# Optimization experiments

Measured on AMD Instinct MI355X. Metric: run time of the kernel, lower is better.

## Reference

```python
import math
import jax, jax.numpy as jnp
import numpy as np

# --- Cayley-Dickson octonion structure constants: e_i * e_j = sign * e_{i XOR j} ---
def _cd_tables(levels=3):
    idx = np.array([[0]]); sgn = np.array([[1]])
    for _ in range(levels):
        n = idx.shape[0]; N = 2 * n
        I = np.zeros((N, N), np.int64); S = np.zeros((N, N), np.int64)
        cj = lambda j: 1 if j == 0 else -1  # conj sign of basis element j
        for i in range(n):
            for j in range(n):
                I[i, j] = idx[i, j];             S[i, j] = sgn[i, j]
                I[i, n + j] = n + idx[j, i];     S[i, n + j] = sgn[j, i]
                I[n + i, j] = n + idx[i, j];     S[n + i, j] = sgn[i, j] * cj(j)
                I[n + i, n + j] = idx[j, i];     S[n + i, n + j] = -cj(j) * sgn[j, i]
        idx, sgn = I, S
    return idx, sgn

_OIDX, _OSGN = _cd_tables()
# Octonion-structured linear: out_i = sum_j SIGN[i,j] * x_j @ W[WIDX[i,j]], WIDX[i,j]=i^j
_WIDX = np.array([[i ^ j for j in range(8)] for i in range(8)], np.int64)
_SIGN = np.array([[_OSGN[j, i ^ j] for j in range(8)] for i in range(8)], np.float32)


def _oct_linear(x, W):
    # x: [B,T,C], W: [8, C/8, C/8]
    B, T, C = x.shape
    Cp = C // 8
    parts = x.reshape(B, T, 8, Cp)
    Weff = jnp.asarray(_SIGN)[:, :, None, None] * W[jnp.asarray(_WIDX)]  # [8,8,Cp,Cp]
    return jnp.einsum('btjp,ijpq->btiq', parts, Weff).reshape(B, T, C)


def _rope(x, cos, sin):
    # x: [B,T,H,D]; consecutive channel pairs form complex numbers
    B, T, H, D = x.shape
    xr = x.reshape(B, T, H, D // 2, 2)
    xe, xo = xr[..., 0], xr[..., 1]
    c = cos[None, :, None, :]
    s = sin[None, :, None, :]
    return jnp.stack([xe * c - xo * s, xe * s + xo * c], axis=-1).reshape(B, T, H, D)


def _forward(x, Wq, Wk, Wv, Wo, mixer_W, mixer_beta, freqs_cos, freqs_sin):
    B, T, C = x.shape
    H = 32; D = C // H
    q = _oct_linear(x, Wq).reshape(B, T, H, D)
    k = _oct_linear(x, Wk).reshape(B, T, H, D)
    v = _oct_linear(x, Wv).reshape(B, T, H, D)
    q = _rope(q, freqs_cos, freqs_sin)
    k = _rope(k, freqs_cos, freqs_sin)
    q = q.transpose(0, 2, 1, 3)  # [B,H,T,D]
    k = k.transpose(0, 2, 1, 3)
    v = v.transpose(0, 2, 1, 3)
    scores = jnp.einsum('bhqd,bhkd->bhqk', q, k) / jnp.sqrt(jnp.float32(D))
    mask = jnp.tril(jnp.ones((T, T), bool))
    scores = jnp.where(mask, scores, jnp.finfo(scores.dtype).min)
    y = jnp.einsum('bhqk,bhkd->bhqd', jax.nn.softmax(scores, axis=-1), v)  # [B,H,T,D]
    # octonion head mixing in groups of 8 heads
    G = H // 8
    yg = y.reshape(B, G, 8, T, D)
    Weff = jnp.asarray(_SIGN)[:, :, None, None] * mixer_W[jnp.asarray(_WIDX)]  # [8,8,D,D]
    mixed = jnp.einsum('bgjtd,ijde->bgite', yg, Weff) * mixer_beta
    y = mixed.reshape(B, H, T, D).transpose(0, 2, 1, 3).reshape(B, T, C)
    return _oct_linear(y, Wo)


def setup_inputs() -> dict:
    key = jax.random.key(0)
    ks = jax.random.split(key, 8)
    B, T, C, H = 1, 2048, 4096, 32
    D = C // H; Cp = C // 8
    x = jax.random.normal(ks[0], (B, T, C), jnp.float32)
    Wq = jax.random.normal(ks[1], (8, Cp, Cp), jnp.float32) * 0.02
    Wk = jax.random.normal(ks[2], (8, Cp, Cp), jnp.float32) * 0.02
    Wv = jax.random.normal(ks[3], (8, Cp, Cp), jnp.float32) * 0.02
    Wo = jax.random.normal(ks[4], (8, Cp, Cp), jnp.float32) * 0.02
    mixer_W = jax.random.normal(ks[5], (8, D, D), jnp.float32) * 0.02
    mixer_beta = jnp.ones((D,), jnp.float32) * np.float32(math.sqrt(3.0 / (2.0 * D)))
    half = D // 2
    inv = 1.0 / (10000.0 ** (np.arange(half) * 2.0 / D))
    ang = np.arange(T)[:, None] * inv[None, :]
    freqs_cos = jnp.asarray(np.cos(ang), jnp.float32)
    freqs_sin = jnp.asarray(np.sin(ang), jnp.float32)
    return dict(x=x, Wq=Wq, Wk=Wk, Wv=Wv, Wo=Wo, mixer_W=mixer_W,
                mixer_beta=mixer_beta, freqs_cos=freqs_cos, freqs_sin=freqs_sin)


def reference(x, Wq, Wk, Wv, Wo, mixer_W, mixer_beta, freqs_cos, freqs_sin):
    return _forward(x, Wq, Wk, Wv, Wo, mixer_W, mixer_beta, freqs_cos, freqs_sin)
```

## Files before the change

kernel.cpp:

```cpp
#include <hip/hip_runtime.h>

typedef float f32x4 __attribute__((ext_vector_type(4)));
typedef __bf16 bf16x8 __attribute__((ext_vector_type(8)));
typedef unsigned short u16;
typedef u16 u16x8 __attribute__((ext_vector_type(8)));

__constant__ float c_osgn[64] = {
  1, 1, 1, 1, 1, 1, 1, 1,
  1,-1, 1,-1, 1,-1,-1, 1,
  1,-1,-1, 1, 1, 1,-1,-1,
  1, 1,-1,-1, 1,-1, 1,-1,
  1,-1,-1,-1,-1, 1, 1, 1,
  1, 1,-1, 1,-1,-1,-1, 1,
  1, 1, 1,-1,-1, 1,-1,-1,
  1,-1, 1, 1,-1,-1, 1,-1
};

__device__ __forceinline__ u16 f2bf(float f) {
  union { float f; unsigned u; } v; v.f = f;
  unsigned u = v.u;
  return (u16)((u + 0x7fffu + ((u >> 16) & 1u)) >> 16);
}
__device__ __forceinline__ float bf2f(u16 h) {
  union { unsigned u; float f; } v; v.u = ((unsigned)h) << 16;
  return v.f;
}

typedef const __attribute__((address_space(1))) void* as1cv;
typedef __attribute__((address_space(3))) void* as3v;
__device__ __forceinline__ void load16_lds(const void* g, void* l) {
  __builtin_amdgcn_global_load_lds((as1cv)g, (as3v)l, 16, 0, 0);
}

__global__ void conv_f32_bf16_vec(const float* __restrict__ src, u16* __restrict__ dst) {
  int i = blockIdx.x * 256 + threadIdx.x;
  float4 v = ((const float4*)src)[i];
  ushort4 o; o.x = f2bf(v.x); o.y = f2bf(v.y); o.z = f2bf(v.z); o.w = f2bf(v.w);
  ((ushort4*)dst)[i] = o;
}

__global__ __launch_bounds__(256) void transpose_w2(const float* __restrict__ W,
                                                    u16* __restrict__ Wt) {
  __shared__ float t[64][65];
  const int w = blockIdx.z, p0 = blockIdx.y * 64, q0 = blockIdx.x * 64;
  const float* src = W + ((long)w * 512 + p0) * 512 + q0;
  const int tid = threadIdx.x;
  const int r = tid >> 2, c0 = (tid & 3) * 16;
#pragma unroll
  for (int j = 0; j < 4; j++) {
    float4 v = *(const float4*)(src + (long)r * 512 + c0 + j * 4);
    t[r][c0 + j * 4 + 0] = v.x; t[r][c0 + j * 4 + 1] = v.y;
    t[r][c0 + j * 4 + 2] = v.z; t[r][c0 + j * 4 + 3] = v.w;
  }
  __syncthreads();
  u16* dst = Wt + ((long)w * 512 + q0) * 512 + p0;
#pragma unroll
  for (int j = 0; j < 2; j++) {
    u16x8 o;
#pragma unroll
    for (int k = 0; k < 8; k++) o[k] = f2bf(t[c0 + j * 8 + k][r]);
    *(u16x8*)(dst + (long)r * 512 + c0 + j * 8) = o;
  }
}

__global__ void transpose_wm(const float* __restrict__ W, const float* __restrict__ beta,
                             u16* __restrict__ Wt) {
  int idx = blockIdx.x * 256 + threadIdx.x;
  int w = idx >> 14, rem = idx & 16383;
  int e = rem >> 7, d = rem & 127;
  Wt[(w << 14) + (e << 7) + d] = f2bf(W[(w << 14) + (d << 7) + e] * beta[e]);
}

template <int MODE>
__global__ __launch_bounds__(256, 3) void oct_gemm128(
    const u16* __restrict__ A, const u16* __restrict__ WtB,
    void* __restrict__ out0, void* __restrict__ out1, void* __restrict__ out2,
    const float* __restrict__ fc, const float* __restrict__ fs,
    int K, int lda, int ldo,
    int slab_shift, int bs_shift, long wslab, long oslab, long acolslab)
{
  __shared__ u16 As[128][64];
  __shared__ u16 Bs[128][64];
  const int NT = K >> 6;
  const int BS = 1 << bs_shift;
  const long wblk = (long)BS * BS;

  const int nwg = gridDim.x * gridDim.y;
  const int lin = blockIdx.y * gridDim.x + blockIdx.x;
  const int swz = (lin & 7) * (nwg >> 3) + (lin >> 3);
  const int bx = swz % gridDim.x, by = swz / gridDim.x;

  const int nglob = bx * 128;
  const int z = nglob >> slab_shift;
  const int np = nglob & ((1 << slab_shift) - 1);
  const int bi = np >> bs_shift;
  const int nsub = np & (BS - 1);
  const int bm = by * 128;
  const u16* Wt = WtB + (long)z * wslab;
  const long acol0 = (long)z * acolslab;

  const int tid = threadIdx.x;
  const int lane = tid & 63, w = tid >> 6;
  const int l15 = lane & 15, lg = lane >> 4;
  const int wm = w >> 1, wn = w & 1;
  const int srow = lane >> 3;
  const int sgr  = (lane & 7) ^ srow;

  f32x4 acc[4][4];
#pragma unroll
  for (int a = 0; a < 4; a++)
#pragma unroll
    for (int b = 0; b < 4; b++) acc[a][b] = f32x4{0.f, 0.f, 0.f, 0.f};

  for (int t = 0; t < NT; ++t) {
    const int k0 = t << 6;
    const int bj = k0 >> bs_shift;
    const int widx = bi ^ bj;
    const unsigned xm = (c_osgn[bj * 8 + widx] < 0.f) ? 0x80008000u : 0u;
    const u16* Wsrc = Wt + (long)widx * wblk + (k0 & (BS - 1));

#pragma unroll
    for (int i = 0; i < 4; i++) {
      const int r = (w * 4 + i) * 8;
      load16_lds(A + (long)(bm + r + srow) * lda + acol0 + k0 + sgr * 8,
                 (void*)&As[r][0]);
    }
#pragma unroll
    for (int i = 0; i < 4; i++) {
      const int r = (w * 4 + i) * 8;
      load16_lds(Wsrc + (long)(nsub + r + srow) * BS + sgr * 8,
                 (void*)&Bs[r][0]);
    }
    __syncthreads();

#pragma unroll
    for (int kk = 0; kk < 64; kk += 32) {
      const int gsw = (((kk >> 3) + lg) ^ (l15 & 7)) * 8;
      uint4 a4[4];
      bf16x8 bF[4];
#pragma unroll
      for (int mt = 0; mt < 4; mt++)
        a4[mt] = *(const uint4*)&As[wm * 64 + mt * 16 + l15][gsw];
      if (xm) {
#pragma unroll
        for (int mt = 0; mt < 4; mt++) {
          a4[mt].x ^= xm; a4[mt].y ^= xm; a4[mt].z ^= xm; a4[mt].w ^= xm;
        }
      }
#pragma unroll
      for (int nt = 0; nt < 4; nt++)
        bF[nt] = *(const bf16x8*)&Bs[wn * 64 + nt * 16 + l15][gsw];
#pragma unroll
      for (int mt = 0; mt < 4; mt++)
#pragma unroll
        for (int nt = 0; nt < 4; nt++)
          acc[mt][nt] = __builtin_amdgcn_mfma_f32_16x16x32_bf16(
              *(const bf16x8*)&a4[mt], bF[nt], acc[mt][nt], 0, 0, 0);
    }
    __syncthreads();
  }

  if constexpr (MODE == 1) {
    if (z == 2) {
      u16* vg = (u16*)out2;
#pragma unroll
      for (int mt = 0; mt < 4; mt++)
#pragma unroll
        for (int nt = 0; nt < 4; nt++)
#pragma unroll
          for (int j = 0; j < 4; j++) {
            const int row = bm + wm * 64 + mt * 16 + 4 * lg + j;
            const int col = np + wn * 64 + nt * 16 + l15;
            vg[(long)row * 4096 + col] = f2bf(acc[mt][nt][j]);
          }
    } else {
      u16* dq = (u16*)(z == 0 ? out0 : out1);
      const int h = np >> 7;
#pragma unroll
      for (int mt = 0; mt < 4; mt++)
#pragma unroll
        for (int nt = 0; nt < 4; nt++) {
          const int d = wn * 64 + nt * 16 + l15;
          const int p = d >> 1;
          const bool ev = (l15 & 1) == 0;
#pragma unroll
          for (int j = 0; j < 4; j++) {
            const int trow = bm + wm * 64 + mt * 16 + 4 * lg + j;
            const float v = acc[mt][nt][j];
            const float sh = __shfl_xor(v, 1);
            const float c = fc[trow * 64 + p];
            const float s = fs[trow * 64 + p];
            const float o = ev ? (v * c - sh * s) : (sh * s + v * c);
            dq[((long)h * 2048 + trow) * 128 + d] = f2bf(o);
          }
        }
    }
  } else {
#pragma unroll
    for (int mt = 0; mt < 4; mt++)
#pragma unroll
      for (int nt = 0; nt < 4; nt++)
#pragma unroll
        for (int j = 0; j < 4; j++) {
          const int row = bm + wm * 64 + mt * 16 + 4 * lg + j;
          const int col = np + wn * 64 + nt * 16 + l15;
          const float v = acc[mt][nt][j];
          if constexpr (MODE == 0)
            ((u16*)out0)[(long)z * oslab + (long)row * ldo + col] = f2bf(v);
          else
            ((float*)out0)[(long)row * ldo + col] = v;
        }
  }
}

__global__ void v_transpose(const u16* __restrict__ vg, u16* __restrict__ vT)
{
  int h = blockIdx.x, t0 = blockIdx.y * 64;
  __shared__ u16 lds[64][136];
  int tid = threadIdx.x;
  int rr = tid >> 4, ch = (tid & 15) * 8;
#pragma unroll
  for (int p = 0; p < 4; p++) {
    int row = p * 16 + rr;
    *(uint4*)&lds[row][ch] = *(const uint4*)(vg + (long)(t0 + row) * 4096 + h * 128 + ch);
  }
  __syncthreads();
  int dd = tid >> 3, tc = (tid & 7) * 8;
#pragma unroll
  for (int p = 0; p < 4; p++) {
    int d = p * 32 + dd;
    u16x8 o;
#pragma unroll
    for (int j = 0; j < 8; j++) o[j] = lds[tc + j][d];
    *(u16x8*)(vT + ((long)h * 128 + d) * 2048 + t0 + tc) = o;
  }
}

__global__ __launch_bounds__(256, 2) void attn3(
    const u16* __restrict__ qR, const u16* __restrict__ kR,
    const u16* __restrict__ vT, u16* __restrict__ y)
{
  const int bid = blockIdx.x;
  const int h = bid & 31;
  const int u = bid >> 5;
  const int qb = (u < 8) ? (u * 2) : (31 - u * 2);
  const int q0 = qb * 128;

  const int tid = threadIdx.x;
  const int lane = tid & 63, w = tid >> 6;
  const int l15 = lane & 15, lg = lane >> 4;

  __shared__ u16 Ks[2][64][128];
  __shared__ u16 Vs[2][128][64];
  __shared__ u16 Ps[4][32][64];

  auto stageK = [&](int kb, int buf) {
    const long kbase = (long)h * 2048 + (long)kb * 64;
#pragma unroll
    for (int i = 0; i < 4; i++) {
      const int j = w * 4 + i;
      const int row = j * 4 + (lane >> 4);
      const int sg = (lane & 15) ^ (row & 7);
      load16_lds(kR + (kbase + row) * 128 + sg * 8, (void*)&Ks[buf][j * 4][0]);
    }
  };
  auto stageV = [&](int kb, int buf) {
    const long vbase = (long)h * 128 * 2048 + (long)kb * 64;
#pragma unroll
    for (int i = 0; i < 4; i++) {
      const int j = w * 4 + i;
      const int row = j * 8 + (lane >> 3);
      const int sg = (lane & 7) ^ (row & 7);
      load16_lds(vT + vbase + (long)row * 2048 + sg * 8, (void*)&Vs[buf][j * 8][0]);
    }
  };

  stageK(0, 0);
  stageV(0, 0);

  bf16x8 aQ[2][4];
#pragma unroll
  for (int rs = 0; rs < 2; rs++) {
    const long qbase = ((long)h * 2048 + q0 + w * 32 + rs * 16 + l15) * 128;
#pragma unroll
    for (int c = 0; c < 4; c++)
      aQ[rs][c] = *(const bf16x8*)(qR + qbase + 32 * c + 8 * lg);
  }

  float m[2][4], lsum[2][4];
  f32x4 Y[2][8];
#pragma unroll
  for (int rs = 0; rs < 2; rs++)
#pragma unroll
    for (int rr = 0; rr < 4; rr++) { m[rs][rr] = -1e30f; lsum[rs][rr] = 0.f; }
#pragma unroll
  for (int rs = 0; rs < 2; rs++)
#pragma unroll
    for (int dt = 0; dt < 8; dt++) Y[rs][dt] = f32x4{0.f, 0.f, 0.f, 0.f};

  const float scale = 0.08838834764831845f;
  const int nkb = 2 * qb + 2;

  for (int kb = 0; kb < nkb; kb++) {
    const int buf = kb & 1;
    const int k0 = kb * 64;
    if (kb + 1 < nkb) { stageK(kb + 1, buf ^ 1); stageV(kb + 1, buf ^ 1); }
    if (kb + 1 < nkb) asm volatile("s_waitcnt vmcnt(8)" ::: "memory");
    else              asm volatile("s_waitcnt vmcnt(0)" ::: "memory");
    __builtin_amdgcn_s_barrier();
    asm volatile("" ::: "memory");

    f32x4 S[2][4];
#pragma unroll
    for (int rs = 0; rs < 2; rs++)
#pragma unroll
      for (int ks = 0; ks < 4; ks++) S[rs][ks] = f32x4{0.f, 0.f, 0.f, 0.f};
#pragma unroll
    for (int c = 0; c < 4; c++) {
      bf16x8 bK[4];
#pragma unroll
      for (int ks = 0; ks < 4; ks++)
        bK[ks] = *(const bf16x8*)&Ks[buf][ks * 16 + l15][(((4 * c + lg) ^ (l15 & 7)) * 8)];
#pragma unroll
      for (int rs = 0; rs < 2; rs++)
#pragma unroll
        for (int ks = 0; ks < 4; ks++)
          S[rs][ks] = __builtin_amdgcn_mfma_f32_16x16x32_bf16(aQ[rs][c], bK[ks], S[rs][ks], 0, 0, 0);
    }

#pragma unroll
    for (int rs = 0; rs < 2; rs++) {
      const int qrow0 = q0 + w * 32 + rs * 16 + 4 * lg;
#pragma unroll
      for (int ks = 0; ks < 4; ks++) {
        const int kg = k0 + ks * 16 + l15;
#pragma unroll
        for (int rr = 0; rr < 4; rr++) {
          float s = S[rs][ks][rr] * scale;
          S[rs][ks][rr] = (kg > qrow0 + rr) ? -1e30f : s;
        }
      }
      float sf[4];
      bool need = false;
#pragma unroll
      for (int rr = 0; rr < 4; rr++) {
        float mx = fmaxf(fmaxf(S[rs][0][rr], S[rs][1][rr]),
                         fmaxf(S[rs][2][rr], S[rs][3][rr]));
#pragma unroll
        for (int off = 1; off < 16; off <<= 1) mx = fmaxf(mx, __shfl_xor(mx, off));
        const bool upd = (mx > m[rs][rr] + 8.f);
        const float mn = upd ? mx : m[rs][rr];
        const float sc = upd ? __expf(m[rs][rr] - mn) : 1.f;
        need |= upd;
        m[rs][rr] = mn;
        float rsum = 0.f;
#pragma unroll
        for (int ks = 0; ks < 4; ks++) {
          float e = __expf(S[rs][ks][rr] - mn);
          S[rs][ks][rr] = e;
          rsum += e;
        }
#pragma unroll
        for (int off = 1; off < 16; off <<= 1) rsum += __shfl_xor(rsum, off);
        lsum[rs][rr] = lsum[rs][rr] * sc + rsum;
        sf[rr] = sc;
      }
      if (__any(need)) {
#pragma unroll
        for (int dt = 0; dt < 8; dt++) {
          f32x4 yv = Y[rs][dt];
          yv[0] *= sf[0]; yv[1] *= sf[1]; yv[2] *= sf[2]; yv[3] *= sf[3];
          Y[rs][dt] = yv;
        }
      }
#pragma unroll
      for (int ks = 0; ks < 4; ks++)
#pragma unroll
        for (int rr = 0; rr < 4; rr++) {
          const int row = rs * 16 + 4 * lg + rr;
          const int G = (2 * ks + (l15 >> 3)) ^ (row & 7);
          Ps[w][row][G * 8 + (l15 & 7)] = f2bf(S[rs][ks][rr]);
        }
    }

#pragma unroll
    for (int kk = 0; kk < 2; kk++) {
      const int pg = ((4 * kk + lg) ^ (l15 & 7)) * 8;
      bf16x8 pF0 = *(const bf16x8*)&Ps[w][l15][pg];
      bf16x8 pF1 = *(const bf16x8*)&Ps[w][16 + l15][pg];
#pragma unroll
      for (int dt = 0; dt < 8; dt++) {
        bf16x8 vF = *(const bf16x8*)&Vs[buf][dt * 16 + l15][pg];
        Y[0][dt] = __builtin_amdgcn_mfma_f32_16x16x32_bf16(pF0, vF, Y[0][dt], 0, 0, 0);
        Y[1][dt] = __builtin_amdgcn_mfma_f32_16x16x32_bf16(pF1, vF, Y[1][dt], 0, 0, 0);
      }
    }
    asm volatile("" ::: "memory");
    __builtin_amdgcn_s_barrier();
    asm volatile("" ::: "memory");
  }

#pragma unroll
  for (int rs = 0; rs < 2; rs++) {
    float inv[4];
#pragma unroll
    for (int rr = 0; rr < 4; rr++) inv[rr] = 1.0f / lsum[rs][rr];
#pragma unroll
    for (int dt = 0; dt < 8; dt++)
#pragma unroll
      for (int rr = 0; rr < 4; rr++)
        y[(long)(q0 + w * 32 + rs * 16 + 4 * lg + rr) * 4096 + h * 128 + dt * 16 + l15] =
            f2bf(Y[rs][dt][rr] * inv[rr]);
  }
}

extern "C" void kernel_launch(void* const* d_in, const int* in_sizes, int n_in,
                              void* d_out, int out_size, void* d_ws, size_t ws_size,
                              hipStream_t stream) {
  const float* x    = (const float*)d_in[0];
  const float* Wq   = (const float*)d_in[1];
  const float* Wk   = (const float*)d_in[2];
  const float* Wv   = (const float*)d_in[3];
  const float* Wo   = (const float*)d_in[4];
  const float* Wm   = (const float*)d_in[5];
  const float* beta = (const float*)d_in[6];
  const float* fc   = (const float*)d_in[7];
  const float* fs   = (const float*)d_in[8];
  float* out = (float*)d_out;

  const long TC = 2048L * 4096L;
  const long WSZ = 8L * 512 * 512;
  u16* ws  = (u16*)d_ws;
  u16* xb  = ws;
  u16* wt  = ws + TC;
  u16* wmt = wt + 4 * WSZ;
  u16* g3  = wmt + 131072L;
  u16* r3  = g3 + 3 * TC;
  u16* yatt = xb;
  u16* ymix = g3;

  conv_f32_bf16_vec<<<TC / 4 / 256, 256, 0, stream>>>(x, xb);
  transpose_w2<<<dim3(8, 8, 8), 256, 0, stream>>>(Wq, wt + 0 * WSZ);
  transpose_w2<<<dim3(8, 8, 8), 256, 0, stream>>>(Wk, wt + 1 * WSZ);
  transpose_w2<<<dim3(8, 8, 8), 256, 0, stream>>>(Wv, wt + 2 * WSZ);
  transpose_w2<<<dim3(8, 8, 8), 256, 0, stream>>>(Wo, wt + 3 * WSZ);
  transpose_wm<<<512, 256, 0, stream>>>(Wm, beta, wmt);

  oct_gemm128<1><<<dim3(96, 16), 256, 0, stream>>>(
      xb, wt, (void*)r3, (void*)(r3 + TC), (void*)g3, fc, fs,
      4096, 4096, 4096, 12, 9, WSZ, 0L, 0L);

  v_transpose<<<dim3(32, 32), 256, 0, stream>>>(g3, r3 + 2 * TC);

  attn3<<<512, 256, 0, stream>>>(r3, r3 + TC, r3 + 2 * TC, yatt);

  oct_gemm128<0><<<dim3(32, 16), 256, 0, stream>>>(
      yatt, wmt, (void*)ymix, nullptr, nullptr, nullptr, nullptr,
      1024, 4096, 4096, 10, 7, 0L, 1024L, 1024L);

  oct_gemm128<2><<<dim3(32, 16), 256, 0, stream>>>(
      ymix, wt + 3 * WSZ, (void*)out, nullptr, nullptr, nullptr, nullptr,
      4096, 4096, 4096, 12, 9, 0L, 0L, 0L);
}
```

Baseline: 472.8 us.

## Fuse V transpose into QKV GEMM epilogue, halve attention query tile, merge weight transposes

The QKV GEMM epilogue for the V slab now transposes the tile through shared memory and writes V directly in [H,D,T] layout. This removes the separate v_transpose kernel and its round trip through global memory. The attention kernel now handles 64 query rows per block, one 16-row slice per wave, across 1024 blocks ordered largest-first, which replaces the paired causal load balancing. The four weight-transpose launches are merged into one. The attention change gives more parallelism and lower register pressure, but each K/V tile loaded is reused by fewer query rows.

```diff
diff --git a/kernel.cpp b/kernel.cpp
--- a/kernel.cpp
+++ b/kernel.cpp
@@ -39,10 +39,16 @@
   ((ushort4*)dst)[i] = o;
 }
 
-__global__ __launch_bounds__(256) void transpose_w2(const float* __restrict__ W,
-                                                    u16* __restrict__ Wt) {
+__global__ __launch_bounds__(256) void transpose_w4(
+    const float* __restrict__ Wq, const float* __restrict__ Wk,
+    const float* __restrict__ Wv, const float* __restrict__ Wo,
+    u16* __restrict__ WtB, long wsz) {
   __shared__ float t[64][65];
-  const int w = blockIdx.z, p0 = blockIdx.y * 64, q0 = blockIdx.x * 64;
+  const int zw = blockIdx.z;
+  const int wsel = zw >> 3, w = zw & 7;
+  const float* W = (wsel == 0) ? Wq : (wsel == 1) ? Wk : (wsel == 2) ? Wv : Wo;
+  u16* Wt = WtB + wsel * wsz;
+  const int p0 = blockIdx.y * 64, q0 = blockIdx.x * 64;
   const float* src = W + ((long)w * 512 + p0) * 512 + q0;
   const int tid = threadIdx.x;
   const int r = tid >> 2, c0 = (tid & 3) * 16;
@@ -79,8 +85,7 @@
     int K, int lda, int ldo,
     int slab_shift, int bs_shift, long wslab, long oslab, long acolslab)
 {
-  __shared__ u16 As[128][64];
-  __shared__ u16 Bs[128][64];
+  __shared__ u16 smem[16384];
   const int NT = K >> 6;
   const int BS = 1 << bs_shift;
   const long wblk = (long)BS * BS;
@@ -123,13 +128,13 @@
     for (int i = 0; i < 4; i++) {
       const int r = (w * 4 + i) * 8;
       load16_lds(A + (long)(bm + r + srow) * lda + acol0 + k0 + sgr * 8,
-                 (void*)&As[r][0]);
+                 (void*)(smem + r * 64));
     }
 #pragma unroll
     for (int i = 0; i < 4; i++) {
       const int r = (w * 4 + i) * 8;
       load16_lds(Wsrc + (long)(nsub + r + srow) * BS + sgr * 8,
-                 (void*)&Bs[r][0]);
+                 (void*)(smem + 8192 + r * 64));
     }
     __syncthreads();
 
@@ -140,7 +145,7 @@
       bf16x8 bF[4];
 #pragma unroll
       for (int mt = 0; mt < 4; mt++)
-        a4[mt] = *(const uint4*)&As[wm * 64 + mt * 16 + l15][gsw];
+        a4[mt] = *(const uint4*)(smem + (wm * 64 + mt * 16 + l15) * 64 + gsw);
       if (xm) {
 #pragma unroll
         for (int mt = 0; mt < 4; mt++) {
@@ -149,7 +154,7 @@
       }
 #pragma unroll
       for (int nt = 0; nt < 4; nt++)
-        bF[nt] = *(const bf16x8*)&Bs[wn * 64 + nt * 16 + l15][gsw];
+        bF[nt] = *(const bf16x8*)(smem + 8192 + (wn * 64 + nt * 16 + l15) * 64 + gsw);
 #pragma unroll
       for (int mt = 0; mt < 4; mt++)
 #pragma unroll
@@ -162,17 +167,30 @@
 
   if constexpr (MODE == 1) {
     if (z == 2) {
-      u16* vg = (u16*)out2;
-#pragma unroll
-      for (int mt = 0; mt < 4; mt++)
-#pragma unroll
-        for (int nt = 0; nt < 4; nt++)
-#pragma unroll
-          for (int j = 0; j < 4; j++) {
-            const int row = bm + wm * 64 + mt * 16 + 4 * lg + j;
-            const int col = np + wn * 64 + nt * 16 + l15;
-            vg[(long)row * 4096 + col] = f2bf(acc[mt][nt][j]);
-          }
+      u16* vT = (u16*)out2;
+      const int h = np >> 7;
+#pragma unroll
+      for (int dh = 0; dh < 2; ++dh) {
+        if (wn == dh) {
+#pragma unroll
+          for (int mt = 0; mt < 4; mt++)
+#pragma unroll
+            for (int nt = 0; nt < 4; nt++)
+#pragma unroll
+              for (int j = 0; j < 4; j++)
+                smem[(nt * 16 + l15) * 144 + wm * 64 + mt * 16 + 4 * lg + j] =
+                    f2bf(acc[mt][nt][j]);
+        }
+        __syncthreads();
+#pragma unroll
+        for (int p = 0; p < 4; ++p) {
+          const int dl = p * 16 + (tid >> 4);
+          const int tt = (tid & 15) * 8;
+          u16x8 o = *(const u16x8*)(smem + dl * 144 + tt);
+          *(u16x8*)(vT + ((long)h * 128 + dh * 64 + dl) * 2048 + bm + tt) = o;
+        }
+        __syncthreads();
+      }
     } else {
       u16* dq = (u16*)(z == 0 ? out0 : out1);
       const int h = np >> 7;
@@ -213,38 +231,14 @@
   }
 }
 
-__global__ void v_transpose(const u16* __restrict__ vg, u16* __restrict__ vT)
-{
-  int h = blockIdx.x, t0 = blockIdx.y * 64;
-  __shared__ u16 lds[64][136];
-  int tid = threadIdx.x;
-  int rr = tid >> 4, ch = (tid & 15) * 8;
-#pragma unroll
-  for (int p = 0; p < 4; p++) {
-    int row = p * 16 + rr;
-    *(uint4*)&lds[row][ch] = *(const uint4*)(vg + (long)(t0 + row) * 4096 + h * 128 + ch);
-  }
-  __syncthreads();
-  int dd = tid >> 3, tc = (tid & 7) * 8;
-#pragma unroll
-  for (int p = 0; p < 4; p++) {
-    int d = p * 32 + dd;
-    u16x8 o;
-#pragma unroll
-    for (int j = 0; j < 8; j++) o[j] = lds[tc + j][d];
-    *(u16x8*)(vT + ((long)h * 128 + d) * 2048 + t0 + tc) = o;
-  }
-}
-
-__global__ __launch_bounds__(256, 2) void attn3(
+__global__ __launch_bounds__(256, 2) void attn4(
     const u16* __restrict__ qR, const u16* __restrict__ kR,
     const u16* __restrict__ vT, u16* __restrict__ y)
 {
   const int bid = blockIdx.x;
   const int h = bid & 31;
-  const int u = bid >> 5;
-  const int qb = (u < 8) ? (u * 2) : (31 - u * 2);
-  const int q0 = qb * 128;
+  const int qb = 31 - (bid >> 5);
+  const int q0 = qb * 64;
 
   const int tid = threadIdx.x;
   const int lane = tid & 63, w = tid >> 6;
@@ -252,7 +246,7 @@
 
   __shared__ u16 Ks[2][64][128];
   __shared__ u16 Vs[2][128][64];
-  __shared__ u16 Ps[4][32][64];
+  __shared__ u16 Ps[4][16][64];
 
   auto stageK = [&](int kb, int buf) {
     const long kbase = (long)h * 2048 + (long)kb * 64;
@@ -278,28 +272,23 @@
   stageK(0, 0);
   stageV(0, 0);
 
-  bf16x8 aQ[2][4];
-#pragma unroll
-  for (int rs = 0; rs < 2; rs++) {
-    const long qbase = ((long)h * 2048 + q0 + w * 32 + rs * 16 + l15) * 128;
+  bf16x8 aQ[4];
+  {
+    const long qbase = ((long)h * 2048 + q0 + w * 16 + l15) * 128;
 #pragma unroll
     for (int c = 0; c < 4; c++)
-      aQ[rs][c] = *(const bf16x8*)(qR + qbase + 32 * c + 8 * lg);
-  }
-
-  float m[2][4], lsum[2][4];
-  f32x4 Y[2][8];
-#pragma unroll
-  for (int rs = 0; rs < 2; rs++)
-#pragma unroll
-    for (int rr = 0; rr < 4; rr++) { m[rs][rr] = -1e30f; lsum[rs][rr] = 0.f; }
-#pragma unroll
-  for (int rs = 0; rs < 2; rs++)
-#pragma unroll
-    for (int dt = 0; dt < 8; dt++) Y[rs][dt] = f32x4{0.f, 0.f, 0.f, 0.f};
+      aQ[c] = *(const bf16x8*)(qR + qbase + 32 * c + 8 * lg);
+  }
+
+  float m[4], lsum[4];
+  f32x4 Y[8];
+#pragma unroll
+  for (int rr = 0; rr < 4; rr++) { m[rr] = -1e30f; lsum[rr] = 0.f; }
+#pragma unroll
+  for (int dt = 0; dt < 8; dt++) Y[dt] = f32x4{0.f, 0.f, 0.f, 0.f};
 
   const float scale = 0.08838834764831845f;
-  const int nkb = 2 * qb + 2;
+  const int nkb = qb + 1;
 
   for (int kb = 0; kb < nkb; kb++) {
     const int buf = kb & 1;
@@ -310,11 +299,9 @@
     __builtin_amdgcn_s_barrier();
     asm volatile("" ::: "memory");
 
-    f32x4 S[2][4];
-#pragma unroll
-    for (int rs = 0; rs < 2; rs++)
-#pragma unroll
-      for (int ks = 0; ks < 4; ks++) S[rs][ks] = f32x4{0.f, 0.f, 0.f, 0.f};
+    f32x4 S[4];
+#pragma unroll
+    for (int ks = 0; ks < 4; ks++) S[ks] = f32x4{0.f, 0.f, 0.f, 0.f};
 #pragma unroll
     for (int c = 0; c < 4; c++) {
       bf16x8 bK[4];
@@ -322,77 +309,71 @@
       for (int ks = 0; ks < 4; ks++)
         bK[ks] = *(const bf16x8*)&Ks[buf][ks * 16 + l15][(((4 * c + lg) ^ (l15 & 7)) * 8)];
 #pragma unroll
-      for (int rs = 0; rs < 2; rs++)
-#pragma unroll
-        for (int ks = 0; ks < 4; ks++)
-          S[rs][ks] = __builtin_amdgcn_mfma_f32_16x16x32_bf16(aQ[rs][c], bK[ks], S[rs][ks], 0, 0, 0);
-    }
-
-#pragma unroll
-    for (int rs = 0; rs < 2; rs++) {
-      const int qrow0 = q0 + w * 32 + rs * 16 + 4 * lg;
+      for (int ks = 0; ks < 4; ks++)
+        S[ks] = __builtin_amdgcn_mfma_f32_16x16x32_bf16(aQ[c], bK[ks], S[ks], 0, 0, 0);
+    }
+
+    {
+      const int qrow0 = q0 + w * 16 + 4 * lg;
 #pragma unroll
       for (int ks = 0; ks < 4; ks++) {
         const int kg = k0 + ks * 16 + l15;
 #pragma unroll
         for (int rr = 0; rr < 4; rr++) {
-          float s = S[rs][ks][rr] * scale;
-          S[rs][ks][rr] = (kg > qrow0 + rr) ? -1e30f : s;
+          float s = S[ks][rr] * scale;
+          S[ks][rr] = (kg > qrow0 + rr) ? -1e30f : s;
         }
       }
       float sf[4];
       bool need = false;
 #pragma unroll
       for (int rr = 0; rr < 4; rr++) {
-        float mx = fmaxf(fmaxf(S[rs][0][rr], S[rs][1][rr]),
-                         fmaxf(S[rs][2][rr], S[rs][3][rr]));
+        float mx = fmaxf(fmaxf(S[0][rr], S[1][rr]), fmaxf(S[2][rr], S[3][rr]));
 #pragma unroll
         for (int off = 1; off < 16; off <<= 1) mx = fmaxf(mx, __shfl_xor(mx, off));
-        const bool upd = (mx > m[rs][rr] + 8.f);
-        const float mn = upd ? mx : m[rs][rr];
-        const float sc = upd ? __expf(m[rs][rr] - mn) : 1.f;
+        const bool upd = (mx > m[rr] + 8.f);
+        const float mn = upd ? mx : m[rr];
+        const float sc = upd ? __expf(m[rr] - mn) : 1.f;
         need |= upd;
-        m[rs][rr] = mn;
+        m[rr] = mn;
         float rsum = 0.f;
 #pragma unroll
         for (int ks = 0; ks < 4; ks++) {
-          float e = __expf(S[rs][ks][rr] - mn);
-          S[rs][ks][rr] = e;
+          float e = __expf(S[ks][rr] - mn);
+          S[ks][rr] = e;
           rsum += e;
         }
 #pragma unroll
         for (int off = 1; off < 16; off <<= 1) rsum += __shfl_xor(rsum, off);
-        lsum[rs][rr] = lsum[rs][rr] * sc + rsum;
+        lsum[rr] = lsum[rr] * sc + rsum;
         sf[rr] = sc;
       }
       if (__any(need)) {
 #pragma unroll
         for (int dt = 0; dt < 8; dt++) {
-          f32x4 yv = Y[rs][dt];
+          f32x4 yv = Y[dt];
           yv[0] *= sf[0]; yv[1] *= sf[1]; yv[2] *= sf[2]; yv[3] *= sf[3];
-          Y[rs][dt] = yv;
+          Y[dt] = yv;
         }
       }
 #pragma unroll
       for (int ks = 0; ks < 4; ks++)
 #pragma unroll
         for (int rr = 0; rr < 4; rr++) {
-          const int row = rs * 16 + 4 * lg + rr;
+          const int row = 4 * lg + rr;
           const int G = (2 * ks + (l15 >> 3)) ^ (row & 7);
-          Ps[w][row][G * 8 + (l15 & 7)] = f2bf(S[rs][ks][rr]);
+          Ps[w][row][G * 8 + (l15 & 7)] = f2bf(S[ks][rr]);
         }
     }
 
 #pragma unroll
     for (int kk = 0; kk < 2; kk++) {
       const int pg = ((4 * kk + lg) ^ (l15 & 7)) * 8;
-      bf16x8 pF0 = *(const bf16x8*)&Ps[w][l15][pg];
-      bf16x8 pF1 = *(const bf16x8*)&Ps[w][16 + l15][pg];
+      bf16x8 pF = *(const bf16x8*)&Ps[w][l15][pg];
 #pragma unroll
       for (int dt = 0; dt < 8; dt++) {
         bf16x8 vF = *(const bf16x8*)&Vs[buf][dt * 16 + l15][pg];
-        Y[0][dt] = __builtin_amdgcn_mfma_f32_16x16x32_bf16(pF0, vF, Y[0][dt], 0, 0, 0);
-        Y[1][dt] = __builtin_amdgcn_mfma_f32_16x16x32_bf16(pF1, vF, Y[1][dt], 0, 0, 0);
+        Y[dt] = __builtin_amdgcn_mfma_f32_16x16x32_bf16(pF, vF, Y[dt], 0, 0, 0);
       }
     }
     asm volatile("" ::: "memory");
@@ -400,18 +381,15 @@
     asm volatile("" ::: "memory");
   }
 
-#pragma unroll
-  for (int rs = 0; rs < 2; rs++) {
-    float inv[4];
-#pragma unroll
-    for (int rr = 0; rr < 4; rr++) inv[rr] = 1.0f / lsum[rs][rr];
-#pragma unroll
-    for (int dt = 0; dt < 8; dt++)
-#pragma unroll
-      for (int rr = 0; rr < 4; rr++)
-        y[(long)(q0 + w * 32 + rs * 16 + 4 * lg + rr) * 4096 + h * 128 + dt * 16 + l15] =
-            f2bf(Y[rs][dt][rr] * inv[rr]);
-  }
+  float inv[4];
+#pragma unroll
+  for (int rr = 0; rr < 4; rr++) inv[rr] = 1.0f / lsum[rr];
+#pragma unroll
+  for (int dt = 0; dt < 8; dt++)
+#pragma unroll
+    for (int rr = 0; rr < 4; rr++)
+      y[(long)(q0 + w * 16 + 4 * lg + rr) * 4096 + h * 128 + dt * 16 + l15] =
+          f2bf(Y[dt][rr] * inv[rr]);
 }
 
 extern "C" void kernel_launch(void* const* d_in, const int* in_sizes, int n_in,
@@ -440,19 +418,14 @@
   u16* ymix = g3;
 
   conv_f32_bf16_vec<<<TC / 4 / 256, 256, 0, stream>>>(x, xb);
-  transpose_w2<<<dim3(8, 8, 8), 256, 0, stream>>>(Wq, wt + 0 * WSZ);
-  transpose_w2<<<dim3(8, 8, 8), 256, 0, stream>>>(Wk, wt + 1 * WSZ);
-  transpose_w2<<<dim3(8, 8, 8), 256, 0, stream>>>(Wv, wt + 2 * WSZ);
-  transpose_w2<<<dim3(8, 8, 8), 256, 0, stream>>>(Wo, wt + 3 * WSZ);
+  transpose_w4<<<dim3(8, 8, 32), 256, 0, stream>>>(Wq, Wk, Wv, Wo, wt, WSZ);
   transpose_wm<<<512, 256, 0, stream>>>(Wm, beta, wmt);
 
   oct_gemm128<1><<<dim3(96, 16), 256, 0, stream>>>(
-      xb, wt, (void*)r3, (void*)(r3 + TC), (void*)g3, fc, fs,
+      xb, wt, (void*)r3, (void*)(r3 + TC), (void*)(r3 + 2 * TC), fc, fs,
       4096, 4096, 4096, 12, 9, WSZ, 0L, 0L);
 
-  v_transpose<<<dim3(32, 32), 256, 0, stream>>>(g3, r3 + 2 * TC);
-
-  attn3<<<512, 256, 0, stream>>>(r3, r3 + TC, r3 + 2 * TC, yatt);
+  attn4<<<1024, 256, 0, stream>>>(r3, r3 + TC, r3 + 2 * TC, yatt);
 
   oct_gemm128<0><<<dim3(32, 16), 256, 0, stream>>>(
       yatt, wmt, (void*)ymix, nullptr, nullptr, nullptr, nullptr,
```

Result: faster. 439.6 us (-7.0%).
